# Optimization experiments

Measured on AMD Instinct MI355X. Metric: run time of the kernel, lower is better.

## Reference

```python
import jax, jax.numpy as jnp
import numpy as np

H_BINS = 64
SIGMA = 0.02
EPS = 1e-6


def setup_inputs() -> dict:
    key = jax.random.key(0)
    x = jax.random.uniform(key, (8, 3, 256, 256), dtype=jnp.float32)
    return {"x": x}


def reference(x):
    h = H_BINS
    L = x.shape[0]
    x = jnp.clip(x, 0.0, 1.0)
    I = x.reshape(L, 3, -1)                      # [L,3,N]
    Iy = jnp.sqrt(jnp.sum(I * I, axis=1) + EPS)  # [L,N] pixel intensity
    logs = jnp.log(I + EPS)                      # [L,3,N]
    # per-channel log-chromaticity: for c=0:(u=l0-l1, v=l0-l2); c=1:(l1-l0, l1-l2); c=2:(l2-l0, l2-l1)
    cu = jnp.array([1, 0, 0])
    cv = jnp.array([2, 2, 1])
    U = logs - logs[:, cu, :]                    # [L,3,N]
    V = logs - logs[:, cv, :]                    # [L,3,N]
    offset = jnp.linspace(-3.0, 3.0, h, dtype=jnp.float32)  # [h]
    inv_s2 = jnp.float32(1.0 / (SIGMA * SIGMA))
    # RBF-like (inverse-quadratic) soft binning kernels: [L,3,N,h]
    Ku = 1.0 / (1.0 + jnp.square(U[..., None] - offset) * inv_s2)
    Kv = 1.0 / (1.0 + jnp.square(V[..., None] - offset) * inv_s2)
    # weighted outer-product reduction over pixels -> [L,3,h,h]
    hists = jnp.einsum('ln,lcnu,lcnv->lcuv', Iy, Ku, Kv)
    # normalize each sample by its total mass
    total = jnp.sum(hists, axis=(1, 2, 3), keepdims=True)
    return hists / (total + EPS)
```

## Files before the change

kernel.cpp:

```cpp
#include <hip/hip_runtime.h>

#define H 64
#define NPIX 65536
#define LBATCH 8
#define LC 24
#define S_CHUNKS 32
#define EPSF 1e-6f

typedef _Float16 h8 __attribute__((ext_vector_type(8)));
typedef float f32x16 __attribute__((ext_vector_type(16)));

__global__ __launch_bounds__(256) void hist_zero(float* __restrict__ out) {
    out[blockIdx.x * 256 + threadIdx.x] = 0.0f;
}

__global__ __launch_bounds__(256, 3) void hist_main(const float* __restrict__ x,
                                                    float* __restrict__ out) {
    __shared__ float sU[4][64];
    __shared__ float sV[4][64];
    __shared__ float sW[4][64];
    __shared__ float sHist[H * H];

    const int tid  = threadIdx.x;
    const int wv   = tid >> 6;
    const int lane = tid & 63;
    const int hf   = lane >> 5;
    const int ln   = lane & 31;
    const int lc   = blockIdx.y;
    const int l    = lc / 3;
    const int c    = lc - 3 * l;

    #pragma unroll
    for (int r = 0; r < 16; r++) sHist[r * 256 + tid] = 0.0f;
    __syncthreads();

    const float step50 = 50.0f * (6.0f / 63.0f);
    const float ou0 = -150.0f + step50 * (float)ln;
    const float ou1 = ou0 + step50 * 32.0f;

    const float* __restrict__ x0p = x + (l * 3 + 0) * NPIX;
    const float* __restrict__ x1p = x + (l * 3 + 1) * NPIX;
    const float* __restrict__ x2p = x + (l * 3 + 2) * NPIX;

    f32x16 acc00, acc01, acc10, acc11;
    #pragma unroll
    for (int i = 0; i < 16; i++) { acc00[i] = 0.0f; acc01[i] = 0.0f; acc10[i] = 0.0f; acc11[i] = 0.0f; }

    const int PB   = NPIX / S_CHUNKS;
    const int base = blockIdx.x * PB;

    for (int t = 0; t < PB / 256; t++) {
        const int p = base + (t * 4 + wv) * 64 + lane;
        float v0 = x0p[p], v1 = x1p[p], v2 = x2p[p];
        v0 = fminf(fmaxf(v0, 0.0f), 1.0f);
        v1 = fminf(fmaxf(v1, 0.0f), 1.0f);
        v2 = fminf(fmaxf(v2, 0.0f), 1.0f);
        const float wgt = sqrtf(fmaf(v0, v0, fmaf(v1, v1, fmaf(v2, v2, EPSF))));
        const float lg0 = logf(v0 + EPSF);
        const float lg1 = logf(v1 + EPSF);
        const float lg2 = logf(v2 + EPSF);
        float U, V;
        if (c == 0)      { U = lg0 - lg1; V = lg0 - lg2; }
        else if (c == 1) { U = lg1 - lg0; V = lg1 - lg2; }
        else             { U = lg2 - lg0; V = lg2 - lg1; }
        sU[wv][lane] = 50.0f * U;
        sV[wv][lane] = 50.0f * V;
        sW[wv][lane] = wgt;

        #pragma unroll
        for (int ks = 0; ks < 4; ks++) {
            const int pk = ks * 16 + hf * 8;
            const float4 ua = *(const float4*)&sU[wv][pk];
            const float4 ub = *(const float4*)&sU[wv][pk + 4];
            const float4 va = *(const float4*)&sV[wv][pk];
            const float4 vb = *(const float4*)&sV[wv][pk + 4];
            const float4 wa = *(const float4*)&sW[wv][pk];
            const float4 wb = *(const float4*)&sW[wv][pk + 4];
            const float uu[8] = {ua.x, ua.y, ua.z, ua.w, ub.x, ub.y, ub.z, ub.w};
            const float vv[8] = {va.x, va.y, va.z, va.w, vb.x, vb.y, vb.z, vb.w};
            const float ww[8] = {wa.x, wa.y, wa.z, wa.w, wb.x, wb.y, wb.z, wb.w};
            h8 a0, a1, b0, b1;
            #pragma unroll
            for (int j = 0; j < 8; j++) {
                const float t0 = uu[j] - ou0;
                const float t1 = uu[j] - ou1;
                const float s0 = vv[j] - ou0;
                const float s1 = vv[j] - ou1;
                a0[j] = (_Float16)(ww[j] * __builtin_amdgcn_rcpf(fmaf(t0, t0, 1.0f)));
                a1[j] = (_Float16)(ww[j] * __builtin_amdgcn_rcpf(fmaf(t1, t1, 1.0f)));
                b0[j] = (_Float16)(__builtin_amdgcn_rcpf(fmaf(s0, s0, 1.0f)));
                b1[j] = (_Float16)(__builtin_amdgcn_rcpf(fmaf(s1, s1, 1.0f)));
            }
            acc00 = __builtin_amdgcn_mfma_f32_32x32x16_f16(a0, b0, acc00, 0, 0, 0);
            acc01 = __builtin_amdgcn_mfma_f32_32x32x16_f16(a0, b1, acc01, 0, 0, 0);
            acc10 = __builtin_amdgcn_mfma_f32_32x32x16_f16(a1, b0, acc10, 0, 0, 0);
            acc11 = __builtin_amdgcn_mfma_f32_32x32x16_f16(a1, b1, acc11, 0, 0, 0);
        }
    }

    #pragma unroll
    for (int r = 0; r < 16; r++) {
        const int row = (r & 3) + 8 * (r >> 2) + 4 * hf;
        atomicAdd(&sHist[row * 64 + ln],             acc00[r]);
        atomicAdd(&sHist[row * 64 + 32 + ln],        acc01[r]);
        atomicAdd(&sHist[(row + 32) * 64 + ln],      acc10[r]);
        atomicAdd(&sHist[(row + 32) * 64 + 32 + ln], acc11[r]);
    }
    __syncthreads();

    float* __restrict__ g = out + lc * (H * H);
    #pragma unroll
    for (int r = 0; r < 16; r++) {
        const int i = r * 256 + tid;
        unsafeAtomicAdd(&g[i], sHist[i]);
    }
}

__global__ __launch_bounds__(256) void hist_finish(float* __restrict__ out) {
    const int l = blockIdx.x;
    float* __restrict__ p = out + l * 3 * H * H;
    float s = 0.0f;
    for (int i = threadIdx.x; i < 3 * H * H; i += 256) s += p[i];
    #pragma unroll
    for (int off = 32; off > 0; off >>= 1) s += __shfl_down(s, off, 64);
    __shared__ float ps[4];
    if ((threadIdx.x & 63) == 0) ps[threadIdx.x >> 6] = s;
    __syncthreads();
    const float T = (ps[0] + ps[1]) + (ps[2] + ps[3]);
    const float inv = 1.0f / (T + EPSF);
    for (int i = threadIdx.x; i < 3 * H * H; i += 256) p[i] *= inv;
}

extern "C" void kernel_launch(void* const* d_in, const int* in_sizes, int n_in,
                              void* d_out, int out_size, void* d_ws, size_t ws_size,
                              hipStream_t stream) {
    const float* x = (const float*)d_in[0];
    float* out = (float*)d_out;

    hipLaunchKernelGGL(hist_zero,   dim3(LC * H * H / 256), dim3(256), 0, stream, out);
    hipLaunchKernelGGL(hist_main,   dim3(S_CHUNKS, LC),     dim3(256), 0, stream, x, out);
    hipLaunchKernelGGL(hist_finish, dim3(LBATCH),           dim3(256), 0, stream, out);
}
```

Baseline: 168.6 us.

## Stage whole pixel chunk in LDS, fast log intrinsics, packed fp16 conversion

```diff
diff --git a/kernel.cpp b/kernel.cpp
--- a/kernel.cpp
+++ b/kernel.cpp
@@ -5,10 +5,17 @@
 #define LBATCH 8
 #define LC 24
 #define S_CHUNKS 32
+#define PB 2048
 #define EPSF 1e-6f
+#define LN2_50 34.6573590f
 
 typedef _Float16 h8 __attribute__((ext_vector_type(8)));
+typedef __fp16   g2 __attribute__((ext_vector_type(2)));
 typedef float f32x16 __attribute__((ext_vector_type(16)));
+union H8u { h8 v8; g2 v2[4]; };
+
+#define KEV(d) __builtin_amdgcn_rcpf(fmaf((d), (d), 1.0f))
+#define PK(a, b) __builtin_amdgcn_cvt_pkrtz((a), (b))
 
 __global__ __launch_bounds__(256) void hist_zero(float* __restrict__ out) {
     out[blockIdx.x * 256 + threadIdx.x] = 0.0f;
@@ -16,9 +23,9 @@
 
 __global__ __launch_bounds__(256, 3) void hist_main(const float* __restrict__ x,
                                                     float* __restrict__ out) {
-    __shared__ float sU[4][64];
-    __shared__ float sV[4][64];
-    __shared__ float sW[4][64];
+    __shared__ float sU[PB];
+    __shared__ float sV[PB];
+    __shared__ float sW[PB];
     __shared__ float sHist[H * H];
 
     const int tid  = threadIdx.x;
@@ -31,71 +38,81 @@
     const int c    = lc - 3 * l;
 
     #pragma unroll
-    for (int r = 0; r < 16; r++) sHist[r * 256 + tid] = 0.0f;
+    for (int r = 0; r < 4; r++)
+        *(float4*)&sHist[(r * 256 + tid) * 4] = make_float4(0.f, 0.f, 0.f, 0.f);
+
+    const float* __restrict__ x0p = x + (l * 3 + 0) * NPIX;
+    const float* __restrict__ x1p = x + (l * 3 + 1) * NPIX;
+    const float* __restrict__ x2p = x + (l * 3 + 2) * NPIX;
+    const int base = blockIdx.x * PB;
+
+    #pragma unroll
+    for (int pass = 0; pass < 2; pass++) {
+        const int ploc = pass * 1024 + tid * 4;
+        const float4 r0 = *(const float4*)&x0p[base + ploc];
+        const float4 r1 = *(const float4*)&x1p[base + ploc];
+        const float4 r2 = *(const float4*)&x2p[base + ploc];
+        float4 U4, V4, W4;
+        #define PREP(E) { \
+            const float v0 = fminf(fmaxf(r0.E, 0.0f), 1.0f); \
+            const float v1 = fminf(fmaxf(r1.E, 0.0f), 1.0f); \
+            const float v2 = fminf(fmaxf(r2.E, 0.0f), 1.0f); \
+            W4.E = __builtin_amdgcn_sqrtf(fmaf(v0, v0, fmaf(v1, v1, fmaf(v2, v2, EPSF)))); \
+            const float lg0 = __builtin_amdgcn_logf(v0 + EPSF); \
+            const float lg1 = __builtin_amdgcn_logf(v1 + EPSF); \
+            const float lg2 = __builtin_amdgcn_logf(v2 + EPSF); \
+            float U, V; \
+            if (c == 0)      { U = lg0 - lg1; V = lg0 - lg2; } \
+            else if (c == 1) { U = lg1 - lg0; V = lg1 - lg2; } \
+            else             { U = lg2 - lg0; V = lg2 - lg1; } \
+            U4.E = LN2_50 * U; V4.E = LN2_50 * V; }
+        PREP(x) PREP(y) PREP(z) PREP(w)
+        #undef PREP
+        *(float4*)&sU[ploc] = U4;
+        *(float4*)&sV[ploc] = V4;
+        *(float4*)&sW[ploc] = W4;
+    }
     __syncthreads();
 
     const float step50 = 50.0f * (6.0f / 63.0f);
     const float ou0 = -150.0f + step50 * (float)ln;
     const float ou1 = ou0 + step50 * 32.0f;
 
-    const float* __restrict__ x0p = x + (l * 3 + 0) * NPIX;
-    const float* __restrict__ x1p = x + (l * 3 + 1) * NPIX;
-    const float* __restrict__ x2p = x + (l * 3 + 2) * NPIX;
-
     f32x16 acc00, acc01, acc10, acc11;
     #pragma unroll
-    for (int i = 0; i < 16; i++) { acc00[i] = 0.0f; acc01[i] = 0.0f; acc10[i] = 0.0f; acc11[i] = 0.0f; }
+    for (int i = 0; i < 16; i++) { acc00[i] = 0.f; acc01[i] = 0.f; acc10[i] = 0.f; acc11[i] = 0.f; }
 
-    const int PB   = NPIX / S_CHUNKS;
-    const int base = blockIdx.x * PB;
-
-    for (int t = 0; t < PB / 256; t++) {
-        const int p = base + (t * 4 + wv) * 64 + lane;
-        float v0 = x0p[p], v1 = x1p[p], v2 = x2p[p];
-        v0 = fminf(fmaxf(v0, 0.0f), 1.0f);
-        v1 = fminf(fmaxf(v1, 0.0f), 1.0f);
-        v2 = fminf(fmaxf(v2, 0.0f), 1.0f);
-        const float wgt = sqrtf(fmaf(v0, v0, fmaf(v1, v1, fmaf(v2, v2, EPSF))));
-        const float lg0 = logf(v0 + EPSF);
-        const float lg1 = logf(v1 + EPSF);
-        const float lg2 = logf(v2 + EPSF);
-        float U, V;
-        if (c == 0)      { U = lg0 - lg1; V = lg0 - lg2; }
-        else if (c == 1) { U = lg1 - lg0; V = lg1 - lg2; }
-        else             { U = lg2 - lg0; V = lg2 - lg1; }
-        sU[wv][lane] = 50.0f * U;
-        sV[wv][lane] = 50.0f * V;
-        sW[wv][lane] = wgt;
-
-        #pragma unroll
-        for (int ks = 0; ks < 4; ks++) {
-            const int pk = ks * 16 + hf * 8;
-            const float4 ua = *(const float4*)&sU[wv][pk];
-            const float4 ub = *(const float4*)&sU[wv][pk + 4];
-            const float4 va = *(const float4*)&sV[wv][pk];
-            const float4 vb = *(const float4*)&sV[wv][pk + 4];
-            const float4 wa = *(const float4*)&sW[wv][pk];
-            const float4 wb = *(const float4*)&sW[wv][pk + 4];
-            const float uu[8] = {ua.x, ua.y, ua.z, ua.w, ub.x, ub.y, ub.z, ub.w};
-            const float vv[8] = {va.x, va.y, va.z, va.w, vb.x, vb.y, vb.z, vb.w};
-            const float ww[8] = {wa.x, wa.y, wa.z, wa.w, wb.x, wb.y, wb.z, wb.w};
-            h8 a0, a1, b0, b1;
-            #pragma unroll
-            for (int j = 0; j < 8; j++) {
-                const float t0 = uu[j] - ou0;
-                const float t1 = uu[j] - ou1;
-                const float s0 = vv[j] - ou0;
-                const float s1 = vv[j] - ou1;
-                a0[j] = (_Float16)(ww[j] * __builtin_amdgcn_rcpf(fmaf(t0, t0, 1.0f)));
-                a1[j] = (_Float16)(ww[j] * __builtin_amdgcn_rcpf(fmaf(t1, t1, 1.0f)));
-                b0[j] = (_Float16)(__builtin_amdgcn_rcpf(fmaf(s0, s0, 1.0f)));
-                b1[j] = (_Float16)(__builtin_amdgcn_rcpf(fmaf(s1, s1, 1.0f)));
-            }
-            acc00 = __builtin_amdgcn_mfma_f32_32x32x16_f16(a0, b0, acc00, 0, 0, 0);
-            acc01 = __builtin_amdgcn_mfma_f32_32x32x16_f16(a0, b1, acc01, 0, 0, 0);
-            acc10 = __builtin_amdgcn_mfma_f32_32x32x16_f16(a1, b0, acc10, 0, 0, 0);
-            acc11 = __builtin_amdgcn_mfma_f32_32x32x16_f16(a1, b1, acc11, 0, 0, 0);
-        }
+    const int wbase = wv * 512;
+    #pragma unroll 2
+    for (int ks = 0; ks < 32; ks++) {
+        const int kb = wbase + ks * 16 + hf * 8;
+        const float4 ua = *(const float4*)&sU[kb];
+        const float4 ub = *(const float4*)&sU[kb + 4];
+        const float4 va = *(const float4*)&sV[kb];
+        const float4 vb = *(const float4*)&sV[kb + 4];
+        const float4 wa = *(const float4*)&sW[kb];
+        const float4 wb = *(const float4*)&sW[kb + 4];
+        H8u A0, A1, B0, B1;
+        A0.v2[0] = PK(wa.x * KEV(ua.x - ou0), wa.y * KEV(ua.y - ou0));
+        A0.v2[1] = PK(wa.z * KEV(ua.z - ou0), wa.w * KEV(ua.w - ou0));
+        A0.v2[2] = PK(wb.x * KEV(ub.x - ou0), wb.y * KEV(ub.y - ou0));
+        A0.v2[3] = PK(wb.z * KEV(ub.z - ou0), wb.w * KEV(ub.w - ou0));
+        A1.v2[0] = PK(wa.x * KEV(ua.x - ou1), wa.y * KEV(ua.y - ou1));
+        A1.v2[1] = PK(wa.z * KEV(ua.z - ou1), wa.w * KEV(ua.w - ou1));
+        A1.v2[2] = PK(wb.x * KEV(ub.x - ou1), wb.y * KEV(ub.y - ou1));
+        A1.v2[3] = PK(wb.z * KEV(ub.z - ou1), wb.w * KEV(ub.w - ou1));
+        B0.v2[0] = PK(KEV(va.x - ou0), KEV(va.y - ou0));
+        B0.v2[1] = PK(KEV(va.z - ou0), KEV(va.w - ou0));
+        B0.v2[2] = PK(KEV(vb.x - ou0), KEV(vb.y - ou0));
+        B0.v2[3] = PK(KEV(vb.z - ou0), KEV(vb.w - ou0));
+        B1.v2[0] = PK(KEV(va.x - ou1), KEV(va.y - ou1));
+        B1.v2[1] = PK(KEV(va.z - ou1), KEV(va.w - ou1));
+        B1.v2[2] = PK(KEV(vb.x - ou1), KEV(vb.y - ou1));
+        B1.v2[3] = PK(KEV(vb.z - ou1), KEV(vb.w - ou1));
+        acc00 = __builtin_amdgcn_mfma_f32_32x32x16_f16(A0.v8, B0.v8, acc00, 0, 0, 0);
+        acc01 = __builtin_amdgcn_mfma_f32_32x32x16_f16(A0.v8, B1.v8, acc01, 0, 0, 0);
+        acc10 = __builtin_amdgcn_mfma_f32_32x32x16_f16(A1.v8, B0.v8, acc10, 0, 0, 0);
+        acc11 = __builtin_amdgcn_mfma_f32_32x32x16_f16(A1.v8, B1.v8, acc11, 0, 0, 0);
     }
 
     #pragma unroll
@@ -120,7 +137,11 @@
     const int l = blockIdx.x;
     float* __restrict__ p = out + l * 3 * H * H;
     float s = 0.0f;
-    for (int i = threadIdx.x; i < 3 * H * H; i += 256) s += p[i];
+    #pragma unroll
+    for (int it = 0; it < 12; it++) {
+        const float4 v = *(const float4*)&p[(it * 256 + threadIdx.x) * 4];
+        s += (v.x + v.y) + (v.z + v.w);
+    }
     #pragma unroll
     for (int off = 32; off > 0; off >>= 1) s += __shfl_down(s, off, 64);
     __shared__ float ps[4];
@@ -128,7 +149,12 @@
     __syncthreads();
     const float T = (ps[0] + ps[1]) + (ps[2] + ps[3]);
     const float inv = 1.0f / (T + EPSF);
-    for (int i = threadIdx.x; i < 3 * H * H; i += 256) p[i] *= inv;
+    #pragma unroll
+    for (int it = 0; it < 12; it++) {
+        float4 v = *(const float4*)&p[(it * 256 + threadIdx.x) * 4];
+        v.x *= inv; v.y *= inv; v.z *= inv; v.w *= inv;
+        *(float4*)&p[(it * 256 + threadIdx.x) * 4] = v;
+    }
 }
 
 extern "C" void kernel_launch(void* const* d_in, const int* in_sizes, int n_in,
```

After: 150.7 us. 1.12x faster.
